# Performance work log

Measured on AMD Instinct MI355X. Metric: run time of the kernel, lower is better.

## Reference

```python
import jax, jax.numpy as jnp
import numpy as np

KERNEL_SIZE = 4
SCALE = 0.5


def setup_inputs() -> dict:
    key = jax.random.key(0)
    k1, k2, k3 = jax.random.split(key, 3)
    M, K, N = 16384, 1024, 4096
    x = jax.random.normal(k1, (M, K), dtype=jnp.float32)
    weight = jax.random.normal(k2, (N, K), dtype=jnp.float32)
    bias = jax.random.normal(k3, (N,), dtype=jnp.float32)
    return {"x": x, "weight": weight, "bias": bias}


def reference(x, weight, bias):
    # y = x @ W^T + b : (M, N)
    y = jnp.einsum('mk,nk->mn', x, weight) + bias[None, :]
    M, N = y.shape
    valid_n = (N // KERNEL_SIZE) * KERNEL_SIZE
    # MaxPool1d(kernel_size, stride=kernel_size): (M, N//k, k) -> max over window
    pooled = jnp.max(y[:, :valid_n].reshape(M, valid_n // KERNEL_SIZE, KERNEL_SIZE), axis=-1)
    # sum over pooled features, then scale -> (M,)
    return jnp.sum(pooled, axis=-1) * SCALE
```

## Files before the change

kernel.cpp:

```cpp
#include <hip/hip_runtime.h>
#include <stdint.h>

#define M_DIM 16384
#define K_DIM 1024
#define N_DIM 4096
#define BM 128
#define BN 128
#define LDSP 40

#define TILE_ELEMS (128 * K_DIM)

#define GBM 256
#define GBN 256
#define NSLAB 32
#define SLOT_E 16384

typedef __bf16 bf16;
typedef __attribute__((ext_vector_type(8))) __bf16 bf16x8;
typedef __attribute__((ext_vector_type(4))) float f32x4;

__device__ __forceinline__ uint32_t pack2_bf16(float a, float b) {
    uint32_t ua = __float_as_uint(a);
    uint32_t ub = __float_as_uint(b);
    ua += 0x7fffu + ((ua >> 16) & 1u);
    ub += 0x7fffu + ((ub >> 16) & 1u);
    return (ua >> 16) | (ub & 0xffff0000u);
}

__global__ __launch_bounds__(256) void convert_pack_kernel(
    const float* __restrict__ x, const float* __restrict__ w,
    bf16* __restrict__ xp, bf16* __restrict__ wp, float* __restrict__ out)
{
    const int t = threadIdx.x;
    const int g = blockIdx.x;
    if (g < (M_DIM / 256)) out[g * 256 + t] = 0.f;

    const int W    = g * 4 + (t >> 6);
    const int lane = t & 63;
    const int tt   = W >> 5;
    const int sub  = W & 31;
    const int rb   = sub & 7;
    const int s0   = (sub >> 3) * 8;

    const float* src; bf16* dst;
    if (tt < (M_DIM / 128)) {
        src = x + (size_t)tt * 128 * K_DIM;
        dst = xp + (size_t)tt * TILE_ELEMS;
    } else {
        const int u = tt - (M_DIM / 128);
        src = w + (size_t)u * 128 * K_DIM;
        dst = wp + (size_t)u * TILE_ELEMS;
    }

    const int lrow = lane & 15, q = lane >> 4;
    const float* rsrc = src + (size_t)(rb * 16 + lrow) * K_DIM + q * 8;
    uint4* dst4 = (uint4*)dst;

    #pragma unroll
    for (int i = 0; i < 8; ++i) {
        const int s = s0 + i;
        float4 a = *(const float4*)(rsrc + s * 32);
        float4 b = *(const float4*)(rsrc + s * 32 + 4);
        uint4 v;
        v.x = pack2_bf16(a.x, a.y);
        v.y = pack2_bf16(a.z, a.w);
        v.z = pack2_bf16(b.x, b.y);
        v.w = pack2_bf16(b.z, b.w);
        dst4[(s * 8 + rb) * 64 + lane] = v;
    }
}


#define BAR() do { asm volatile("" ::: "memory"); \
                   __builtin_amdgcn_s_barrier();  \
                   asm volatile("" ::: "memory"); } while (0)
#define VMCNT4() asm volatile("s_waitcnt vmcnt(4)" ::: "memory")
#define VMCNT0() asm volatile("s_waitcnt vmcnt(0)" ::: "memory")

#define STG(sl, ch, gsrc) \
    __builtin_amdgcn_global_load_lds( \
        (const __attribute__((address_space(1))) unsigned int*)(gsrc), \
        (__attribute__((address_space(3))) unsigned int*)&sm[(((sl) & 3) * SLOT_E) + (ch) * 4096 + w * 512], \
        16, 0, 0)

#define STG_A(t) do { STG(t, 0, Ag + (size_t)(t) * 4096 + toff); \
                      STG(t, 1, Ag + TILE_ELEMS + (size_t)(t) * 4096 + toff); } while (0)
#define STG_B(t) do { STG(t, 2, Bg + (size_t)(t) * 4096 + toff); \
                      STG(t, 3, Bg + TILE_ELEMS + (size_t)(t) * 4096 + toff); } while (0)

#define RD4(dst, base) do { \
    _Pragma("unroll") \
    for (int _i = 0; _i < 4; ++_i) \
        dst[_i] = *(const bf16x8*)&sm[(base) + _i * 512]; \
} while (0)

#define MFMA16X(Aset, Bset, IB) do { \
    __builtin_amdgcn_s_setprio(1); \
    _Pragma("unroll") \
    for (int ii = 0; ii < 4; ++ii) \
        _Pragma("unroll") \
        for (int jj = 0; jj < 4; ++jj) \
            acc[(IB) + ii][jj] = __builtin_amdgcn_mfma_f32_16x16x32_bf16( \
                Aset[ii], Bset[jj], acc[(IB) + ii][jj], 0, 0, 0); \
    __builtin_amdgcn_s_setprio(0); \
} while (0)

#define SLAB(s, CUR, NXT) do { \
    if ((s) + 2 < NSLAB) STG_A((s) + 2); \
    RD4(Ahi, (((s) & 3) * SLOT_E) + aOff + 2048); \
    MFMA16X(Alo##CUR, Bv##CUR, 0); \
    if ((s) + 2 < NSLAB) STG_B((s) + 2); \
    if ((s) == NSLAB - 2) { VMCNT0(); } else if ((s) < NSLAB - 2) { VMCNT4(); } \
    BAR(); \
    if ((s) + 1 < NSLAB) { \
        RD4(Alo##NXT, ((((s) + 1) & 3) * SLOT_E) + aOff); \
        RD4(Bv##NXT,  ((((s) + 1) & 3) * SLOT_E) + bOff); \
    } \
    MFMA16X(Ahi, Bv##CUR, 4); \
} while (0)

__global__ __launch_bounds__(512, 2) void gemm_pool_ring_kernel(
    const bf16* __restrict__ xp, const bf16* __restrict__ wp,
    const float* __restrict__ bias, float* __restrict__ out)
{
    __shared__ bf16 sm[4 * SLOT_E];

    const int b  = blockIdx.x;
    const int bx = b & (N_DIM / GBN - 1);
    const int by = b >> 4;

    const int tid  = threadIdx.x;
    const int lane = tid & 63;
    const int w    = tid >> 6;
    const int wm   = w >> 2;
    const int wn   = w & 3;
    const int lr   = lane & 15;
    const int quad = lane >> 4;
    const int toff = tid * 8;

    const bf16* __restrict__ Ag = xp + (size_t)(2 * by) * TILE_ELEMS;
    const bf16* __restrict__ Bg = wp + (size_t)(2 * bx) * TILE_ELEMS;

    const int aOff = wm * 4096 + lane * 8;
    const int bOff = 8192 + (wn >> 1) * 4096 + (wn & 1) * 2048 + lane * 8;

    f32x4 acc[8][4] = {};
    bf16x8 AloA[4], AloB[4], Ahi[4], BvA[4], BvB[4];

    STG_A(0); STG_B(0);
    STG_A(1); STG_B(1);
    VMCNT4(); BAR();
    RD4(AloA, aOff);
    RD4(BvA,  bOff);

    #pragma unroll
    for (int sp = 0; sp < NSLAB / 2; ++sp) {
        SLAB(2 * sp,     A, B);
        SLAB(2 * sp + 1, B, A);
    }

    float bv[4];
    #pragma unroll
    for (int j = 0; j < 4; ++j)
        bv[j] = bias[bx * GBN + wn * 64 + j * 16 + lr];

    #pragma unroll
    for (int i = 0; i < 8; ++i) {
        float rs[4] = {0.f, 0.f, 0.f, 0.f};
        #pragma unroll
        for (int j = 0; j < 4; ++j) {
            #pragma unroll
            for (int r = 0; r < 4; ++r) {
                float v = acc[i][j][r] + bv[j];
                v = fmaxf(v, __shfl_xor(v, 1, 64));
                v = fmaxf(v, __shfl_xor(v, 2, 64));
                rs[r] += v;
            }
        }
        #pragma unroll
        for (int r = 0; r < 4; ++r) {
            rs[r] += __shfl_xor(rs[r], 4, 64);
            rs[r] += __shfl_xor(rs[r], 8, 64);
        }
        if (lr == 0) {
            const int row = by * GBM + wm * 128 + i * 16 + quad * 4;
            #pragma unroll
            for (int r = 0; r < 4; ++r)
                atomicAdd(&out[row + r], rs[r] * 0.5f);
        }
    }
}

__global__ __launch_bounds__(256) void fused_linear_pool_kernel(
    const float* __restrict__ x, const float* __restrict__ wt,
    const float* __restrict__ bias, float* __restrict__ out)
{
    __shared__ uint32_t sA[BM * LDSP / 2];
    __shared__ uint32_t sB[BN * LDSP / 2];

    const int tid = threadIdx.x;
    const int bx = blockIdx.x;
    const int by = blockIdx.y;

    const float* Abase = x  + (size_t)by * BM * K_DIM;
    const float* Bbase = wt + (size_t)bx * BN * K_DIM;

    const int lane = tid & 63;
    const int wave = tid >> 6;
    const int wm = wave >> 1;
    const int wn = wave & 1;
    const int lr = lane & 15;
    const int quad = lane >> 4;

    const int srow  = tid >> 2;
    const int scol  = (tid & 3) * 8;
    const int swidx = (tid & 3) * 4;

    f32x4 acc[4][4] = {};

    for (int kt = 0; kt < K_DIM; kt += 32) {
        #pragma unroll
        for (int p = 0; p < 2; ++p) {
            const int r = srow + p * 64;
            const float4* ga = (const float4*)(Abase + (size_t)r * K_DIM + kt + scol);
            const float4* gb = (const float4*)(Bbase + (size_t)r * K_DIM + kt + scol);
            float4 a0 = ga[0], a1 = ga[1], b0 = gb[0], b1 = gb[1];
            uint4 wa;
            wa.x = pack2_bf16(a0.x, a0.y); wa.y = pack2_bf16(a0.z, a0.w);
            wa.z = pack2_bf16(a1.x, a1.y); wa.w = pack2_bf16(a1.z, a1.w);
            *(uint4*)&sA[r * (LDSP / 2) + swidx] = wa;
            uint4 wbv;
            wbv.x = pack2_bf16(b0.x, b0.y); wbv.y = pack2_bf16(b0.z, b0.w);
            wbv.z = pack2_bf16(b1.x, b1.y); wbv.w = pack2_bf16(b1.z, b1.w);
            *(uint4*)&sB[r * (LDSP / 2) + swidx] = wbv;
        }
        __syncthreads();

        bf16x8 af[4], bfr[4];
        #pragma unroll
        for (int i = 0; i < 4; ++i)
            af[i] = *(const bf16x8*)((const bf16*)sA + (wm * 64 + i * 16 + lr) * LDSP + quad * 8);
        #pragma unroll
        for (int j = 0; j < 4; ++j)
            bfr[j] = *(const bf16x8*)((const bf16*)sB + (wn * 64 + j * 16 + lr) * LDSP + quad * 8);

        #pragma unroll
        for (int i = 0; i < 4; ++i)
            #pragma unroll
            for (int j = 0; j < 4; ++j)
                acc[i][j] = __builtin_amdgcn_mfma_f32_16x16x32_bf16(af[i], bfr[j], acc[i][j], 0, 0, 0);
        __syncthreads();
    }

    float bv[4];
    #pragma unroll
    for (int j = 0; j < 4; ++j)
        bv[j] = bias[bx * BN + wn * 64 + j * 16 + lr];

    #pragma unroll
    for (int i = 0; i < 4; ++i) {
        float rsum[4] = {0.f, 0.f, 0.f, 0.f};
        #pragma unroll
        for (int j = 0; j < 4; ++j) {
            #pragma unroll
            for (int r = 0; r < 4; ++r) {
                float t = acc[i][j][r] + bv[j];
                t = fmaxf(t, __shfl_xor(t, 1, 64));
                t = fmaxf(t, __shfl_xor(t, 2, 64));
                t += __shfl_xor(t, 4, 64);
                t += __shfl_xor(t, 8, 64);
                rsum[r] += t;
            }
        }
        if (lr == 0) {
            const int row = by * BM + wm * 64 + i * 16 + quad * 4;
            #pragma unroll
            for (int r = 0; r < 4; ++r)
                atomicAdd(&out[row + r], rsum[r] * 0.5f);
        }
    }
}

extern "C" void kernel_launch(void* const* d_in, const int* in_sizes, int n_in,
                              void* d_out, int out_size, void* d_ws, size_t ws_size,
                              hipStream_t stream) {
    const float* x  = (const float*)d_in[0];
    const float* wt = (const float*)d_in[1];
    const float* bs = (const float*)d_in[2];
    float* out = (float*)d_out;

    const size_t xe = (size_t)M_DIM * K_DIM;
    const size_t we = (size_t)N_DIM * K_DIM;
    const size_t need = (xe + we) * sizeof(bf16);

    if (ws_size >= need) {
        bf16* xp = (bf16*)d_ws;
        bf16* wp = xp + xe;
        convert_pack_kernel<<<1280, 256, 0, stream>>>(x, wt, xp, wp, out);
        gemm_pool_ring_kernel<<<(M_DIM / GBM) * (N_DIM / GBN), 512, 0, stream>>>(xp, wp, bs, out);
    } else {
        hipMemsetAsync(out, 0, (size_t)out_size * sizeof(float), stream);
        dim3 grid(N_DIM / BN, M_DIM / BM);
        fused_linear_pool_kernel<<<grid, 256, 0, stream>>>(x, wt, bs, out);
    }
}
```

Before: 245.4 us.

## Switch GEMM-pool kernel from 16x16x32 to 32x32x16 bf16 MFMA tiles

Replaces the 16x16x32 MFMA micro-tiles with 32x32x16 MFMA, so each wave issues 8 larger MFMAs per half-slab instead of 16. The LDS fragment addressing and the accumulator layout are rewritten to match, and the max-pool/sum epilogue is remapped to the 32x32 output layout with an extra shuffle stage. The aim is fewer MFMA issues and LDS reads per FLOP, at the risk of wrong results if the fragment addressing does not match the packed layout.

```diff
diff --git a/kernel.cpp b/kernel.cpp
--- a/kernel.cpp
+++ b/kernel.cpp
@@ -18,6 +18,7 @@
 typedef __bf16 bf16;
 typedef __attribute__((ext_vector_type(8))) __bf16 bf16x8;
 typedef __attribute__((ext_vector_type(4))) float f32x4;
+typedef __attribute__((ext_vector_type(16))) float f32x16;
 
 __device__ __forceinline__ uint32_t pack2_bf16(float a, float b) {
     uint32_t ua = __float_as_uint(a);
@@ -88,42 +89,53 @@
 #define STG_B(t) do { STG(t, 2, Bg + (size_t)(t) * 4096 + toff); \
                       STG(t, 3, Bg + TILE_ELEMS + (size_t)(t) * 4096 + toff); } while (0)
 
-#define RD4(dst, base) do { \
+#define SLB(s) (((s) & 3) * 32768)
+
+#define RDA(dst, slotBytes, KO) do { \
     _Pragma("unroll") \
     for (int _i = 0; _i < 4; ++_i) \
-        dst[_i] = *(const bf16x8*)&sm[(base) + _i * 512]; \
+        dst[_i] = *(const bf16x8*)(smB + (slotBytes) + aFB + _i * 2048 + (KO) * 512); \
 } while (0)
 
-#define MFMA16X(Aset, Bset, IB) do { \
+#define RDB(dst, slotBytes) do { \
+    _Pragma("unroll") \
+    for (int _c = 0; _c < 2; ++_c) \
+        _Pragma("unroll") \
+        for (int _k = 0; _k < 2; ++_k) \
+            dst[_c * 2 + _k] = *(const bf16x8*)(smB + (slotBytes) + bFB + _c * 2048 + _k * 512); \
+} while (0)
+
+#define MFMA8(Aset, Bset, KO) do { \
     __builtin_amdgcn_s_setprio(1); \
     _Pragma("unroll") \
-    for (int ii = 0; ii < 4; ++ii) \
+    for (int _r = 0; _r < 4; ++_r) \
         _Pragma("unroll") \
-        for (int jj = 0; jj < 4; ++jj) \
-            acc[(IB) + ii][jj] = __builtin_amdgcn_mfma_f32_16x16x32_bf16( \
-                Aset[ii], Bset[jj], acc[(IB) + ii][jj], 0, 0, 0); \
+        for (int _c = 0; _c < 2; ++_c) \
+            acc[_r][_c] = __builtin_amdgcn_mfma_f32_32x32x16_bf16( \
+                Aset[_r], Bset[_c * 2 + (KO)], acc[_r][_c], 0, 0, 0); \
     __builtin_amdgcn_s_setprio(0); \
 } while (0)
 
 #define SLAB(s, CUR, NXT) do { \
     if ((s) + 2 < NSLAB) STG_A((s) + 2); \
-    RD4(Ahi, (((s) & 3) * SLOT_E) + aOff + 2048); \
-    MFMA16X(Alo##CUR, Bv##CUR, 0); \
+    RDA(Ahi, SLB(s), 1); \
+    MFMA8(Alo##CUR, Bv##CUR, 0); \
     if ((s) + 2 < NSLAB) STG_B((s) + 2); \
     if ((s) == NSLAB - 2) { VMCNT0(); } else if ((s) < NSLAB - 2) { VMCNT4(); } \
     BAR(); \
     if ((s) + 1 < NSLAB) { \
-        RD4(Alo##NXT, ((((s) + 1) & 3) * SLOT_E) + aOff); \
-        RD4(Bv##NXT,  ((((s) + 1) & 3) * SLOT_E) + bOff); \
+        RDA(Alo##NXT, SLB((s) + 1), 0); \
+        RDB(Bv##NXT,  SLB((s) + 1)); \
     } \
-    MFMA16X(Ahi, Bv##CUR, 4); \
+    MFMA8(Ahi, Bv##CUR, 1); \
 } while (0)
 
-__global__ __launch_bounds__(512, 2) void gemm_pool_ring_kernel(
+__global__ __launch_bounds__(512, 2) void gemm_pool_ring32_kernel(
     const bf16* __restrict__ xp, const bf16* __restrict__ wp,
     const float* __restrict__ bias, float* __restrict__ out)
 {
     __shared__ bf16 sm[4 * SLOT_E];
+    const char* smB = (const char*)sm;
 
     const int b  = blockIdx.x;
     const int bx = b & (N_DIM / GBN - 1);
@@ -134,24 +146,26 @@
     const int w    = tid >> 6;
     const int wm   = w >> 2;
     const int wn   = w & 3;
-    const int lr   = lane & 15;
-    const int quad = lane >> 4;
     const int toff = tid * 8;
+
+    const int h8 = lane >> 5;
+    const int c5 = lane & 31;
 
     const bf16* __restrict__ Ag = xp + (size_t)(2 * by) * TILE_ELEMS;
     const bf16* __restrict__ Bg = wp + (size_t)(2 * bx) * TILE_ELEMS;
 
-    const int aOff = wm * 4096 + lane * 8;
-    const int bOff = 8192 + (wn >> 1) * 4096 + (wn & 1) * 2048 + lane * 8;
-
-    f32x4 acc[8][4] = {};
+    const int fragLane = (c5 >> 4) * 1024 + h8 * 256 + (c5 & 15) * 16;
+    const int aFB = wm * 8192 + fragLane;
+    const int bFB = 16384 + (wn >> 1) * 8192 + (wn & 1) * 4096 + fragLane;
+
+    f32x16 acc[4][2] = {};
     bf16x8 AloA[4], AloB[4], Ahi[4], BvA[4], BvB[4];
 
     STG_A(0); STG_B(0);
     STG_A(1); STG_B(1);
     VMCNT4(); BAR();
-    RD4(AloA, aOff);
-    RD4(BvA,  bOff);
+    RDA(AloA, SLB(0), 0);
+    RDB(BvA,  SLB(0));
 
     #pragma unroll
     for (int sp = 0; sp < NSLAB / 2; ++sp) {
@@ -159,34 +173,39 @@
         SLAB(2 * sp + 1, B, A);
     }
 
-    float bv[4];
-    #pragma unroll
-    for (int j = 0; j < 4; ++j)
-        bv[j] = bias[bx * GBN + wn * 64 + j * 16 + lr];
-
-    #pragma unroll
-    for (int i = 0; i < 8; ++i) {
-        float rs[4] = {0.f, 0.f, 0.f, 0.f};
-        #pragma unroll
-        for (int j = 0; j < 4; ++j) {
-            #pragma unroll
-            for (int r = 0; r < 4; ++r) {
-                float v = acc[i][j][r] + bv[j];
+    float bvv[2];
+    #pragma unroll
+    for (int c = 0; c < 2; ++c)
+        bvv[c] = bias[bx * GBN + wn * 64 + c * 32 + c5];
+
+    #pragma unroll
+    for (int i = 0; i < 4; ++i) {
+        float rs[16];
+        #pragma unroll
+        for (int r = 0; r < 16; ++r) rs[r] = 0.f;
+        #pragma unroll
+        for (int c = 0; c < 2; ++c) {
+            #pragma unroll
+            for (int r = 0; r < 16; ++r) {
+                float v = acc[i][c][r] + bvv[c];
                 v = fmaxf(v, __shfl_xor(v, 1, 64));
                 v = fmaxf(v, __shfl_xor(v, 2, 64));
                 rs[r] += v;
             }
         }
         #pragma unroll
-        for (int r = 0; r < 4; ++r) {
+        for (int r = 0; r < 16; ++r) {
             rs[r] += __shfl_xor(rs[r], 4, 64);
             rs[r] += __shfl_xor(rs[r], 8, 64);
-        }
-        if (lr == 0) {
-            const int row = by * GBM + wm * 128 + i * 16 + quad * 4;
-            #pragma unroll
-            for (int r = 0; r < 4; ++r)
-                atomicAdd(&out[row + r], rs[r] * 0.5f);
+            rs[r] += __shfl_xor(rs[r], 16, 64);
+        }
+        if (c5 == 0) {
+            #pragma unroll
+            for (int r = 0; r < 16; ++r) {
+                const int row = by * GBM + wm * 128 + i * 32
+                              + (r & 3) + 8 * (r >> 2) + 4 * h8;
+                atomicAdd(&out[row], rs[r] * 0.5f);
+            }
         }
     }
 }
@@ -297,7 +316,7 @@
         bf16* xp = (bf16*)d_ws;
         bf16* wp = xp + xe;
         convert_pack_kernel<<<1280, 256, 0, stream>>>(x, wt, xp, wp, out);
-        gemm_pool_ring_kernel<<<(M_DIM / GBM) * (N_DIM / GBN), 512, 0, stream>>>(xp, wp, bs, out);
+        gemm_pool_ring32_kernel<<<(M_DIM / GBM) * (N_DIM / GBN), 512, 0, stream>>>(xp, wp, bs, out);
     } else {
         hipMemsetAsync(out, 0, (size_t)out_size * sizeof(float), stream);
         dim3 grid(N_DIM / BN, M_DIM / BM);
```

Measured after the change: 307.1 us. 25.2% more time.

## Shrink GEMM-pool block tile to 128x128 with 4 waves per block

Applied to the files above, without the earlier changes.

Reduces the block tile from 256x256 (512 threads, 8 waves) to 128x128 (256 threads, 4 waves), halves the LDS ring slot size, and rewrites the staging/read offsets and MFMA loops so each wave computes a 64x64 sub-tile. This gives four times as many blocks and smaller LDS use, which should raise occupancy and CU load balance. In exchange, reuse of each loaded tile drops, so global/L2 traffic per FLOP roughly doubles, and more atomic adds hit the output.

```diff
diff --git a/kernel.cpp b/kernel.cpp
--- a/kernel.cpp
+++ b/kernel.cpp
@@ -10,10 +10,10 @@
 
 #define TILE_ELEMS (128 * K_DIM)
 
-#define GBM 256
-#define GBN 256
+#define GBM 128
+#define GBN 128
 #define NSLAB 32
-#define SLOT_E 16384
+#define SLOT_E 8192
 
 typedef __bf16 bf16;
 typedef __attribute__((ext_vector_type(8))) __bf16 bf16x8;
@@ -77,16 +77,23 @@
 #define VMCNT4() asm volatile("s_waitcnt vmcnt(4)" ::: "memory")
 #define VMCNT0() asm volatile("s_waitcnt vmcnt(0)" ::: "memory")
 
-#define STG(sl, ch, gsrc) \
+#define STG(sl, part, gsrc) \
     __builtin_amdgcn_global_load_lds( \
         (const __attribute__((address_space(1))) unsigned int*)(gsrc), \
-        (__attribute__((address_space(3))) unsigned int*)&sm[(((sl) & 3) * SLOT_E) + (ch) * 4096 + w * 512], \
+        (__attribute__((address_space(3))) unsigned int*)&sm[(((sl) & 3) * SLOT_E) + (part) * 2048 + w * 512], \
         16, 0, 0)
 
 #define STG_A(t) do { STG(t, 0, Ag + (size_t)(t) * 4096 + toff); \
-                      STG(t, 1, Ag + TILE_ELEMS + (size_t)(t) * 4096 + toff); } while (0)
+                      STG(t, 1, Ag + (size_t)(t) * 4096 + 2048 + toff); } while (0)
 #define STG_B(t) do { STG(t, 2, Bg + (size_t)(t) * 4096 + toff); \
-                      STG(t, 3, Bg + TILE_ELEMS + (size_t)(t) * 4096 + toff); } while (0)
+                      STG(t, 3, Bg + (size_t)(t) * 4096 + 2048 + toff); } while (0)
+
+#define SLB(s) (((s) & 3) * SLOT_E)
+
+#define RD2(dst, base) do { \
+    dst[0] = *(const bf16x8*)&sm[(base)]; \
+    dst[1] = *(const bf16x8*)&sm[(base) + 512]; \
+} while (0)
 
 #define RD4(dst, base) do { \
     _Pragma("unroll") \
@@ -94,10 +101,10 @@
         dst[_i] = *(const bf16x8*)&sm[(base) + _i * 512]; \
 } while (0)
 
-#define MFMA16X(Aset, Bset, IB) do { \
+#define MFMA8(Aset, Bset, IB) do { \
     __builtin_amdgcn_s_setprio(1); \
     _Pragma("unroll") \
-    for (int ii = 0; ii < 4; ++ii) \
+    for (int ii = 0; ii < 2; ++ii) \
         _Pragma("unroll") \
         for (int jj = 0; jj < 4; ++jj) \
             acc[(IB) + ii][jj] = __builtin_amdgcn_mfma_f32_16x16x32_bf16( \
@@ -107,19 +114,19 @@
 
 #define SLAB(s, CUR, NXT) do { \
     if ((s) + 2 < NSLAB) STG_A((s) + 2); \
-    RD4(Ahi, (((s) & 3) * SLOT_E) + aOff + 2048); \
-    MFMA16X(Alo##CUR, Bv##CUR, 0); \
+    RD2(Ahi, SLB(s) + aOff + 1024); \
+    MFMA8(Alo##CUR, Bv##CUR, 0); \
     if ((s) + 2 < NSLAB) STG_B((s) + 2); \
     if ((s) == NSLAB - 2) { VMCNT0(); } else if ((s) < NSLAB - 2) { VMCNT4(); } \
     BAR(); \
     if ((s) + 1 < NSLAB) { \
-        RD4(Alo##NXT, ((((s) + 1) & 3) * SLOT_E) + aOff); \
-        RD4(Bv##NXT,  ((((s) + 1) & 3) * SLOT_E) + bOff); \
+        RD2(Alo##NXT, SLB((s) + 1) + aOff); \
+        RD4(Bv##NXT,  SLB((s) + 1) + bOff); \
     } \
-    MFMA16X(Ahi, Bv##CUR, 4); \
+    MFMA8(Ahi, Bv##CUR, 2); \
 } while (0)
 
-__global__ __launch_bounds__(512, 2) void gemm_pool_ring_kernel(
+__global__ __launch_bounds__(256) void gemm_pool_q_kernel(
     const bf16* __restrict__ xp, const bf16* __restrict__ wp,
     const float* __restrict__ bias, float* __restrict__ out)
 {
@@ -127,30 +134,30 @@
 
     const int b  = blockIdx.x;
     const int bx = b & (N_DIM / GBN - 1);
-    const int by = b >> 4;
+    const int by = b >> 5;
 
     const int tid  = threadIdx.x;
     const int lane = tid & 63;
     const int w    = tid >> 6;
-    const int wm   = w >> 2;
-    const int wn   = w & 3;
+    const int wm   = w >> 1;
+    const int wn   = w & 1;
     const int lr   = lane & 15;
     const int quad = lane >> 4;
     const int toff = tid * 8;
 
-    const bf16* __restrict__ Ag = xp + (size_t)(2 * by) * TILE_ELEMS;
-    const bf16* __restrict__ Bg = wp + (size_t)(2 * bx) * TILE_ELEMS;
-
-    const int aOff = wm * 4096 + lane * 8;
-    const int bOff = 8192 + (wn >> 1) * 4096 + (wn & 1) * 2048 + lane * 8;
-
-    f32x4 acc[8][4] = {};
-    bf16x8 AloA[4], AloB[4], Ahi[4], BvA[4], BvB[4];
+    const bf16* __restrict__ Ag = xp + (size_t)by * TILE_ELEMS;
+    const bf16* __restrict__ Bg = wp + (size_t)bx * TILE_ELEMS;
+
+    const int aOff = wm * 2048 + lane * 8;
+    const int bOff = 4096 + wn * 2048 + lane * 8;
+
+    f32x4 acc[4][4] = {};
+    bf16x8 AloA[2], AloB[2], Ahi[2], BvA[4], BvB[4];
 
     STG_A(0); STG_B(0);
     STG_A(1); STG_B(1);
     VMCNT4(); BAR();
-    RD4(AloA, aOff);
+    RD2(AloA, aOff);
     RD4(BvA,  bOff);
 
     #pragma unroll
@@ -165,7 +172,7 @@
         bv[j] = bias[bx * GBN + wn * 64 + j * 16 + lr];
 
     #pragma unroll
-    for (int i = 0; i < 8; ++i) {
+    for (int i = 0; i < 4; ++i) {
         float rs[4] = {0.f, 0.f, 0.f, 0.f};
         #pragma unroll
         for (int j = 0; j < 4; ++j) {
@@ -183,7 +190,7 @@
             rs[r] += __shfl_xor(rs[r], 8, 64);
         }
         if (lr == 0) {
-            const int row = by * GBM + wm * 128 + i * 16 + quad * 4;
+            const int row = by * GBM + wm * 64 + i * 16 + quad * 4;
             #pragma unroll
             for (int r = 0; r < 4; ++r)
                 atomicAdd(&out[row + r], rs[r] * 0.5f);
@@ -297,7 +304,7 @@
         bf16* xp = (bf16*)d_ws;
         bf16* wp = xp + xe;
         convert_pack_kernel<<<1280, 256, 0, stream>>>(x, wt, xp, wp, out);
-        gemm_pool_ring_kernel<<<(M_DIM / GBM) * (N_DIM / GBN), 512, 0, stream>>>(xp, wp, bs, out);
+        gemm_pool_q_kernel<<<(M_DIM / GBM) * (N_DIM / GBN), 256, 0, stream>>>(xp, wp, bs, out);
     } else {
         hipMemsetAsync(out, 0, (size_t)out_size * sizeof(float), stream);
         dim3 grid(N_DIM / BN, M_DIM / BM);
```

Measured after the change: 265.1 us. 1.08x slower.
